# Kernel tuning notes

Hardware: AMD Instinct MI355X
Metric: run time of the kernel (lower is better)

Reference implementation:

```python
import jax, jax.numpy as jnp
import numpy as np

B, C, H, W = 4, 256, 128, 128
K = 3
BN = max(16, C // 4)  # 64
PAD = K // 2
EPS = 1e-5


def conv2d(x, w, b=None, pad=0):
    out = jax.lax.conv_general_dilated(
        x, w, (1, 1), [(pad, pad), (pad, pad)],
        dimension_numbers=("NCHW", "OIHW", "NCHW"))
    if b is not None:
        out = out + b[None, :, None, None]
    return out


def deform_conv2d(z, offset, mask, w, b):
    # torchvision modulated deform conv v2: offset [B,2*K*K,H,W] interleaved (dy,dx),
    # mask [B,K*K,H,W], kernel positions row-major, stride 1, pad PAD.
    Bz, Cb, Hz, Wz = z.shape
    K2 = K * K
    off = offset.reshape(Bz, K2, 2, Hz, Wz)
    ky, kx = jnp.meshgrid(jnp.arange(K), jnp.arange(K), indexing="ij")
    # sampling positions py/px: [B, K2, H, W]
    py = off[:, :, 0] + jnp.arange(Hz)[None, None, :, None] + (ky.reshape(K2) - PAD)[None, :, None, None]
    px = off[:, :, 1] + jnp.arange(Wz)[None, None, None, :] + (kx.reshape(K2) - PAD)[None, :, None, None]
    y0 = jnp.floor(py)
    x0 = jnp.floor(px)
    wy1 = py - y0  # frac weights
    wx1 = px - x0
    z_flat = z.reshape(Bz, Cb, Hz * Wz)

    def gather(yy, xx, wgt):
        valid = (yy >= 0) & (yy < Hz) & (xx >= 0) & (xx < Wz)
        yc = jnp.clip(yy, 0, Hz - 1).astype(jnp.int32)
        xc = jnp.clip(xx, 0, Wz - 1).astype(jnp.int32)
        idx = (yc * Wz + xc).reshape(Bz, K2 * Hz * Wz)
        g = jnp.take_along_axis(z_flat, idx[:, None, :], axis=2)  # [B, Cb, K2*H*W]
        g = g.reshape(Bz, Cb, K2, Hz, Wz)
        return g * (wgt * valid.astype(z.dtype))[:, None]

    val = (gather(y0, x0, (1 - wy1) * (1 - wx1))
           + gather(y0, x0 + 1, (1 - wy1) * wx1)
           + gather(y0 + 1, x0, wy1 * (1 - wx1))
           + gather(y0 + 1, x0 + 1, wy1 * wx1))
    val = val * mask[:, None]  # modulate: [B, Cb, K2, H, W]
    out = jnp.einsum("bckhw,ock->bohw", val, w.reshape(w.shape[0], Cb, K2))
    return out + b[None, :, None, None]


def setup_inputs() -> dict:
    key = jax.random.key(0)
    ks = jax.random.split(key, 11)
    s = 0.05
    return {
        "x": jax.random.normal(ks[0], (B, C, H, W), jnp.float32),
        "down_w": jax.random.normal(ks[1], (BN, C, 1, 1), jnp.float32) * s,
        "off_w": jax.random.normal(ks[2], (2 * K * K, BN, 3, 3), jnp.float32) * s,
        "off_b": jax.random.normal(ks[3], (2 * K * K,), jnp.float32) * s,
        "mask_w": jax.random.normal(ks[4], (K * K, BN, 3, 3), jnp.float32) * s,
        "mask_b": jax.random.normal(ks[5], (K * K,), jnp.float32) * s,
        "def_w": jax.random.normal(ks[6], (BN, BN, K, K), jnp.float32) * s,
        "def_b": jax.random.normal(ks[7], (BN,), jnp.float32) * s,
        "up_w": jax.random.normal(ks[8], (C, BN, 1, 1), jnp.float32) * s,
        "gamma": jnp.ones((C,), jnp.float32),
        "beta": jnp.zeros((C,), jnp.float32),
    }


def reference(x, down_w, off_w, off_b, mask_w, mask_b, def_w, def_b, up_w, gamma, beta):
    z = conv2d(x, down_w)                               # 1x1 down: [B, BN, H, W]
    offset = conv2d(z, off_w, off_b, pad=1)             # [B, 18, H, W]
    mask = jax.nn.sigmoid(conv2d(z, mask_w, mask_b, pad=1))  # [B, 9, H, W]
    z = deform_conv2d(z, offset, mask, def_w, def_b)    # [B, BN, H, W]
    z = conv2d(z, up_w)                                 # 1x1 up: [B, C, H, W]
    y = x + z
    # BatchNorm2d in training mode: batch statistics over (B, H, W), biased var
    mean = jnp.mean(y, axis=(0, 2, 3), keepdims=True)
    var = jnp.var(y, axis=(0, 2, 3), keepdims=True)
    yh = (y - mean) * jax.lax.rsqrt(var + EPS)
    yh = yh * gamma[None, :, None, None] + beta[None, :, None, None]
    return yh * jax.nn.sigmoid(yh)  # SiLU
```

## Files before the change

### kernel.cpp

```cpp
#include <hip/hip_runtime.h>
#include <hip/hip_bf16.h>


typedef __attribute__((ext_vector_type(8))) short bf16x8;
typedef __attribute__((ext_vector_type(4))) short bf16x4;
typedef __attribute__((ext_vector_type(4))) float f32x4;

#define HW   16384
#define CC   256
#define BNC  64

#define WS_STATS   0
#define WS_SS      262144
#define WS_FD      264192
#define WS_FOM     296960
#define WS_FDEF    333824
#define WS_FUP     407552
#define WS_ZBF     440320
#define WS_OM      8828928

__device__ __forceinline__ short f2b(float f) {
    unsigned u = __float_as_uint(f);
    unsigned r = (u + 0x7FFFu + ((u >> 16) & 1u)) >> 16;
    return (short)r;
}
__device__ __forceinline__ float b2f(short s) {
    return __uint_as_float(((unsigned)(unsigned short)s) << 16);
}

__global__ void k_prep(const float* __restrict__ down_w, const float* __restrict__ off_w,
                       const float* __restrict__ mask_w, const float* __restrict__ def_w,
                       const float* __restrict__ up_w, char* __restrict__ ws) {
    int g = blockIdx.x * 256 + threadIdx.x;
    int row = g >> 6, lane = g & 63;
    if (row >= 172) return;
    int l15 = lane & 15, q = lane >> 4;
    short vals[8];
    short* dst;
    if (row < 32) {
        int nt = row >> 3, kk = row & 7;
        int n = nt * 16 + l15;
        for (int j = 0; j < 8; ++j) {
            int c = kk * 32 + q * 8 + j;
            vals[j] = f2b(down_w[n * 256 + c]);
        }
        dst = (short*)(ws + WS_FD) + row * 512 + lane * 8;
    } else if (row < 68) {
        int r = row - 32; int nt = r / 18, kk = r % 18;
        int n = nt * 16 + l15;
        for (int j = 0; j < 8; ++j) {
            int kap = kk * 32 + q * 8 + j; int k = kap >> 6, c = kap & 63;
            float v = 0.f;
            if (n < 18)      v = off_w[(n * 64 + c) * 9 + k];
            else if (n < 27) v = mask_w[((n - 18) * 64 + c) * 9 + k];
            vals[j] = f2b(v);
        }
        dst = (short*)(ws + WS_FOM) + r * 512 + lane * 8;
    } else if (row < 140) {
        int r = row - 68; int nt = r / 18, kk = r % 18;
        int n = nt * 16 + l15;
        int u = kk * 4 + q, k = u >> 3;
        for (int j = 0; j < 8; ++j) {
            int c = (u & 7) * 8 + j;
            vals[j] = f2b(def_w[(n * 64 + c) * 9 + k]);
        }
        dst = (short*)(ws + WS_FDEF) + r * 512 + lane * 8;
    } else {
        int r = row - 140; int nt = r >> 1, kk = r & 1;
        int o = nt * 16 + l15;
        for (int j = 0; j < 8; ++j) {
            int c = kk * 32 + q * 8 + j;
            vals[j] = f2b(up_w[o * 64 + c]);
        }
        dst = (short*)(ws + WS_FUP) + r * 512 + lane * 8;
    }
    for (int j = 0; j < 8; ++j) dst[j] = vals[j];
}

__global__ __launch_bounds__(256) void k_down(const float* __restrict__ x,
                                              const short* __restrict__ wfd,
                                              short* __restrict__ zbf) {
    __shared__ __align__(16) short xl[64 * 264];
    int blk = blockIdx.x;
    int b = blk >> 8;
    int hw0 = (blk & 255) * 64;
    int t = threadIdx.x;
    const float* xb = x + (size_t)b * CC * HW + hw0;
    int px = t & 63, w = t >> 6;
    for (int h = 0; h < 8; ++h) {
        int c0 = h * 32 + w * 8;
        bf16x8 pk;
        #pragma unroll
        for (int j = 0; j < 8; ++j)
            pk[j] = f2b(xb[(size_t)(c0 + j) * HW + px]);
        *(bf16x8*)(&xl[px * 264 + c0]) = pk;
    }
    __syncthreads();
    int lane = t & 63, wv = t >> 6;
    int l15 = lane & 15, q = lane >> 4;
    bf16x8 A[8];
    const short* xrow = &xl[(wv * 16 + l15) * 264];
    for (int kk = 0; kk < 8; ++kk)
        A[kk] = *(const bf16x8*)(xrow + kk * 32 + q * 8);
    const bf16x8* Bp = (const bf16x8*)wfd;
    size_t obase = ((size_t)b * HW + hw0 + wv * 16) * 64;
    for (int nt = 0; nt < 4; ++nt) {
        f32x4 acc = {0.f, 0.f, 0.f, 0.f};
        for (int kk = 0; kk < 8; ++kk) {
            bf16x8 Bf = Bp[(nt * 8 + kk) * 64 + lane];
            acc = __builtin_amdgcn_mfma_f32_16x16x32_bf16(A[kk], Bf, acc, 0, 0, 0);
        }
        int n = nt * 16 + l15;
        for (int r = 0; r < 4; ++r) {
            int prow = q * 4 + r;
            zbf[obase + (size_t)prow * 64 + n] = f2b(acc[r]);
        }
    }
}

__global__ __launch_bounds__(256) void k_offmask(const short* __restrict__ zbf,
                                                 const short* __restrict__ wfom,
                                                 const float* __restrict__ off_b,
                                                 const float* __restrict__ mask_b,
                                                 float* __restrict__ om) {
    int blk = blockIdx.x;
    int b = blk >> 8;
    int hw0 = (blk & 255) * 64;
    int y = hw0 >> 7, x0 = hw0 & 127;
    int t = threadIdx.x, lane = t & 63, wv = t >> 6;
    int l15 = lane & 15, q = lane >> 4;
    int xx0 = x0 + wv * 16 + l15;
    const short* zb = zbf + (size_t)b * HW * 64;
    f32x4 acc0 = {0, 0, 0, 0}, acc1 = {0, 0, 0, 0};
    const bf16x8* Bp = (const bf16x8*)wfom;
    for (int kk = 0; kk < 18; ++kk) {
        int k = kk >> 1;
        int yy = y + (k / 3) - 1;
        int xx = xx0 + (k % 3) - 1;
        int c0 = (kk & 1) * 32 + q * 8;
        bf16x8 A = {0, 0, 0, 0, 0, 0, 0, 0};
        if (yy >= 0 && yy < 128 && xx >= 0 && xx < 128)
            A = *(const bf16x8*)(zb + ((size_t)(yy * 128 + xx)) * 64 + c0);
        bf16x8 B0 = Bp[kk * 64 + lane];
        bf16x8 B1 = Bp[(18 + kk) * 64 + lane];
        acc0 = __builtin_amdgcn_mfma_f32_16x16x32_bf16(A, B0, acc0, 0, 0, 0);
        acc1 = __builtin_amdgcn_mfma_f32_16x16x32_bf16(A, B1, acc1, 0, 0, 0);
    }
    float* omb = om + ((size_t)b * HW + hw0 + wv * 16) * 27;
    for (int half = 0; half < 2; ++half) {
        f32x4 acc = half ? acc1 : acc0;
        int n = half * 16 + l15;
        if (n < 27) {
            for (int r = 0; r < 4; ++r) {
                int prow = q * 4 + r;
                float v = acc[r];
                if (n < 18) v += off_b[n];
                else { v += mask_b[n - 18]; v = 1.f / (1.f + __expf(-v)); }
                omb[prow * 27 + n] = v;
            }
        }
    }
}

__global__ __launch_bounds__(256) void k_deform_up(
        const short* __restrict__ zbf, const float* __restrict__ om,
        const short* __restrict__ wfdef, const float* __restrict__ def_b,
        const short* __restrict__ wfup, const float* __restrict__ x,
        float* __restrict__ yout, float* __restrict__ stats) {
    __shared__ __align__(16) short valA[1152 * 8];
    __shared__ __align__(16) char  uSm[4608];
    int4*   pAi4 = (int4*)uSm;
    float4* pAw4 = (float4*)(uSm + 2304);
    short*  z2t  = (short*)uSm;

    int blk = blockIdx.x;
    int b = blk >> 10;
    int tile = blk & 1023;
    int oy = tile >> 3, xt = (tile & 7) << 4;
    int hw0 = oy * 128 + xt;
    int t = threadIdx.x;
    const short* zbs = zbf + (size_t)b * HW * 64;
    if (t < 144) {
        int px = t / 9, k = t % 9;
        int ox = xt + px;
        const float* p = om + ((size_t)b * HW + hw0 + px) * 27;
        float dy = p[2 * k], dx = p[2 * k + 1], m = p[18 + k];
        float py  = (float)oy + (float)(k / 3 - 1) + dy;
        float pxf = (float)ox + (float)(k % 3 - 1) + dx;
        float fy = floorf(py), fx = floorf(pxf);
        int iy = (int)fy, ix = (int)fx;
        float wy = py - fy, wx = pxf - fx;
        float ww[4] = { (1.f - wy) * (1.f - wx) * m, (1.f - wy) * wx * m,
                        wy * (1.f - wx) * m,          wy * wx * m };
        int ys[2] = {iy, iy + 1}, xs[2] = {ix, ix + 1};
        int   ri[4]; float rw[4];
        for (int ci = 0; ci < 4; ++ci) {
            int cy = ys[ci >> 1], cx = xs[ci & 1];
            bool v = (cy >= 0 && cy < 128 && cx >= 0 && cx < 128);
            ri[ci] = v ? (cy * 128 + cx) * 64 : 0;
            rw[ci] = v ? ww[ci] : 0.f;
        }
        pAi4[t] = make_int4(ri[0], ri[1], ri[2], ri[3]);
        pAw4[t] = make_float4(rw[0], rw[1], rw[2], rw[3]);
    }
    __syncthreads();
    for (int it = 0; it < 5; ++it) {
        int s = t + it * 256;
        if (s < 1152) {
            int px = s / 72;
            int u  = s - px * 72;
            int k = u >> 3, cg = u & 7;
            int task = px * 9 + k;
            int4   idx = pAi4[task];
            float4 wt  = pAw4[task];
            int   ii[4] = { idx.x, idx.y, idx.z, idx.w };
            float wwt[4] = { wt.x, wt.y, wt.z, wt.w };
            int cgs = cg * 8;
            float acc[8] = {0.f, 0.f, 0.f, 0.f, 0.f, 0.f, 0.f, 0.f};
            #pragma unroll
            for (int ci = 0; ci < 4; ++ci) {
                float w = wwt[ci];
                int4 d = *(const int4*)(zbs + ii[ci] + cgs);
                int dp[4] = { d.x, d.y, d.z, d.w };
                #pragma unroll
                for (int p = 0; p < 4; ++p) {
                    float lo = __uint_as_float((unsigned)dp[p] << 16);
                    float hi = __uint_as_float((unsigned)dp[p] & 0xffff0000u);
                    acc[2 * p]     += w * lo;
                    acc[2 * p + 1] += w * hi;
                }
            }
            bf16x8 out;
            #pragma unroll
            for (int j = 0; j < 8; ++j) out[j] = f2b(acc[j]);
            int unit = u * 16 + (px ^ (u & 15));
            *(bf16x8*)(&valA[unit * 8]) = out;
        }
    }
    __syncthreads();
    int lane = t & 63, wv = t >> 6;
    int l15 = lane & 15, q = lane >> 4;
    {
        f32x4 acc = {0, 0, 0, 0};
        const bf16x8* Bp = (const bf16x8*)wfdef;
        for (int kk = 0; kk < 18; ++kk) {
            int u = kk * 4 + q;
            int unit = u * 16 + (l15 ^ (u & 15));
            bf16x8 A  = *(const bf16x8*)(&valA[unit * 8]);
            bf16x8 Bf = Bp[(wv * 18 + kk) * 64 + lane];
            acc = __builtin_amdgcn_mfma_f32_16x16x32_bf16(A, Bf, acc, 0, 0, 0);
        }
        int n = wv * 16 + l15;
        float bias = def_b[n];
        for (int r = 0; r < 4; ++r) {
            int prow = q * 4 + r;
            z2t[prow * 64 + (n ^ ((prow & 7) << 3))] = f2b(acc[r] + bias);
        }
    }
    __syncthreads();
    int rsw = (l15 & 7) << 3;
    bf16x8 A0 = *(const bf16x8*)&z2t[l15 * 64 + ((q * 8) ^ rsw)];
    bf16x8 A1 = *(const bf16x8*)&z2t[l15 * 64 + ((32 + q * 8) ^ rsw)];
    const bf16x8* Bu = (const bf16x8*)wfup;
    int bucket = blk & 127;
    size_t xybase = (size_t)b * CC * HW + hw0 + q * 4;
    #pragma unroll
    for (int nt = 0; nt < 4; ++nt) {
        int ont = wv * 4 + nt;
        f32x4 acc = {0, 0, 0, 0};
        acc = __builtin_amdgcn_mfma_f32_16x16x32_bf16(A0, Bu[(ont * 2 + 0) * 64 + lane], acc, 0, 0, 0);
        acc = __builtin_amdgcn_mfma_f32_16x16x32_bf16(A1, Bu[(ont * 2 + 1) * 64 + lane], acc, 0, 0, 0);
        int o = ont * 16 + l15;
        size_t pb = xybase + (size_t)o * HW;
        float4 xv = *(const float4*)(x + pb);
        float v0 = acc[0] + xv.x;
        float v1 = acc[1] + xv.y;
        float v2 = acc[2] + xv.z;
        float v3 = acc[3] + xv.w;
        *(float4*)(yout + pb) = make_float4(v0, v1, v2, v3);
        float s  = v0 + v1 + v2 + v3;
        float s2 = v0 * v0 + v1 * v1 + v2 * v2 + v3 * v3;
        s  += __shfl_xor(s, 16);  s  += __shfl_xor(s, 32);
        s2 += __shfl_xor(s2, 16); s2 += __shfl_xor(s2, 32);
        if (q == 0) {
            atomicAdd(&stats[bucket * 512 + o], s);
            atomicAdd(&stats[bucket * 512 + 256 + o], s2);
        }
    }
}

__global__ void k_stats(const float* __restrict__ stats, const float* __restrict__ gamma,
                        const float* __restrict__ beta, float* __restrict__ ss) {
    int o = threadIdx.x;
    float a0 = 0.f, a1 = 0.f, a2 = 0.f, a3 = 0.f;
    float b0 = 0.f, b1 = 0.f, b2 = 0.f, b3 = 0.f;
    #pragma unroll 4
    for (int u = 0; u < 128; u += 4) {
        a0 += stats[(u + 0) * 512 + o];  b0 += stats[(u + 0) * 512 + 256 + o];
        a1 += stats[(u + 1) * 512 + o];  b1 += stats[(u + 1) * 512 + 256 + o];
        a2 += stats[(u + 2) * 512 + o];  b2 += stats[(u + 2) * 512 + 256 + o];
        a3 += stats[(u + 3) * 512 + o];  b3 += stats[(u + 3) * 512 + 256 + o];
    }
    float s = (a0 + a1) + (a2 + a3);
    float s2 = (b0 + b1) + (b2 + b3);
    float mean = s * (1.f / 65536.f);
    float var  = s2 * (1.f / 65536.f) - mean * mean;
    float rs = rsqrtf(var + 1e-5f);
    float sc = gamma[o] * rs;
    ss[o]       = sc;
    ss[256 + o] = beta[o] - mean * sc;
}

__global__ __launch_bounds__(256) void k_bn(float* __restrict__ y, const float* __restrict__ ss) {
    int g = blockIdx.x * 256 + threadIdx.x;
    int o = (g >> 10) & 255;
    float sc = ss[o], sh = ss[256 + o];
    float4* p = (float4*)y + (size_t)g * 4;
    for (int i = 0; i < 4; ++i) {
        float4 v = p[i];
        float vf[4] = { v.x, v.y, v.z, v.w };
        for (int j = 0; j < 4; ++j) {
            float h = vf[j] * sc + sh;
            vf[j] = h / (1.f + __expf(-h));
        }
        p[i] = make_float4(vf[0], vf[1], vf[2], vf[3]);
    }
}

extern "C" void kernel_launch(void* const* d_in, const int* in_sizes, int n_in,
                              void* d_out, int out_size, void* d_ws, size_t ws_size,
                              hipStream_t stream) {
    const float* x      = (const float*)d_in[0];
    const float* down_w = (const float*)d_in[1];
    const float* off_w  = (const float*)d_in[2];
    const float* off_b  = (const float*)d_in[3];
    const float* mask_w = (const float*)d_in[4];
    const float* mask_b = (const float*)d_in[5];
    const float* def_w  = (const float*)d_in[6];
    const float* def_b  = (const float*)d_in[7];
    const float* up_w   = (const float*)d_in[8];
    const float* gamma  = (const float*)d_in[9];
    const float* beta   = (const float*)d_in[10];
    char* ws = (char*)d_ws;
    float* stats = (float*)(ws + WS_STATS);
    float* ss    = (float*)(ws + WS_SS);
    short* wfd   = (short*)(ws + WS_FD);
    short* wfom  = (short*)(ws + WS_FOM);
    short* wfdef = (short*)(ws + WS_FDEF);
    short* wfup  = (short*)(ws + WS_FUP);
    short* zbf   = (short*)(ws + WS_ZBF);
    float* om    = (float*)(ws + WS_OM);
    float* y     = (float*)d_out;

    hipMemsetAsync(stats, 0, 128 * 512 * sizeof(float), stream);
    hipLaunchKernelGGL(k_prep,      dim3(43),   dim3(256), 0, stream, down_w, off_w, mask_w, def_w, up_w, ws);
    hipLaunchKernelGGL(k_down,      dim3(1024), dim3(256), 0, stream, x, wfd, zbf);
    hipLaunchKernelGGL(k_offmask,   dim3(1024), dim3(256), 0, stream, zbf, wfom, off_b, mask_b, om);
    hipLaunchKernelGGL(k_deform_up, dim3(4096), dim3(256), 0, stream, zbf, om, wfdef, def_b, wfup, x, y, stats);
    hipLaunchKernelGGL(k_stats,     dim3(1),    dim3(256), 0, stream, stats, gamma, beta, ss);
    hipLaunchKernelGGL(k_bn,        dim3(4096), dim3(256), 0, stream, y, ss);
}
```

Measured before the change: 230.1 us.

## Enlarge deform+up tile to 64 pixels per block with sequential sub-tiles

Each k_deform_up block now covers 64 consecutive pixels of a row instead of 16. It runs the sampling, gather and deform MFMA phases over four 16-pixel sub-tiles, stores all results into a 64x64 z2t buffer, then does the 1x1 up-projection over four row tiles. The grid drops from 4096 to 1024 blocks. The aim is to amortise block launch, weight fragment loads and per-block setup over more pixels and to give longer contiguous x/y row accesses. The costs are less parallelism, more LDS per block because buffers are no longer aliased, and serialised barriers within each block that may reduce latency hiding.

Result: slower. 244.4 us (+6.2%).

```diff
diff --git a/kernel.cpp b/kernel.cpp
--- a/kernel.cpp
+++ b/kernel.cpp
@@ -167,124 +167,130 @@
         const short* __restrict__ wfdef, const float* __restrict__ def_b,
         const short* __restrict__ wfup, const float* __restrict__ x,
         float* __restrict__ yout, float* __restrict__ stats) {
-    __shared__ __align__(16) short valA[1152 * 8];
-    __shared__ __align__(16) char  uSm[4608];
-    int4*   pAi4 = (int4*)uSm;
-    float4* pAw4 = (float4*)(uSm + 2304);
-    short*  z2t  = (short*)uSm;
+    __shared__ __align__(16) short  valA[1152 * 8];
+    __shared__ __align__(16) short  z2t[64 * 64];
+    __shared__ __align__(16) int4   pAi4[144];
+    __shared__ __align__(16) float4 pAw4[144];
 
     int blk = blockIdx.x;
-    int b = blk >> 10;
-    int tile = blk & 1023;
-    int oy = tile >> 3, xt = (tile & 7) << 4;
-    int hw0 = oy * 128 + xt;
+    int b = blk >> 8;
+    int tile = blk & 255;
+    int oy = tile >> 1;
+    int x0 = (tile & 1) << 6;
+    int hw0 = oy * 128 + x0;
     int t = threadIdx.x;
-    const short* zbs = zbf + (size_t)b * HW * 64;
-    if (t < 144) {
-        int px = t / 9, k = t % 9;
-        int ox = xt + px;
-        const float* p = om + ((size_t)b * HW + hw0 + px) * 27;
-        float dy = p[2 * k], dx = p[2 * k + 1], m = p[18 + k];
-        float py  = (float)oy + (float)(k / 3 - 1) + dy;
-        float pxf = (float)ox + (float)(k % 3 - 1) + dx;
-        float fy = floorf(py), fx = floorf(pxf);
-        int iy = (int)fy, ix = (int)fx;
-        float wy = py - fy, wx = pxf - fx;
-        float ww[4] = { (1.f - wy) * (1.f - wx) * m, (1.f - wy) * wx * m,
-                        wy * (1.f - wx) * m,          wy * wx * m };
-        int ys[2] = {iy, iy + 1}, xs[2] = {ix, ix + 1};
-        int   ri[4]; float rw[4];
-        for (int ci = 0; ci < 4; ++ci) {
-            int cy = ys[ci >> 1], cx = xs[ci & 1];
-            bool v = (cy >= 0 && cy < 128 && cx >= 0 && cx < 128);
-            ri[ci] = v ? (cy * 128 + cx) * 64 : 0;
-            rw[ci] = v ? ww[ci] : 0.f;
-        }
-        pAi4[t] = make_int4(ri[0], ri[1], ri[2], ri[3]);
-        pAw4[t] = make_float4(rw[0], rw[1], rw[2], rw[3]);
-    }
-    __syncthreads();
-    for (int it = 0; it < 5; ++it) {
-        int s = t + it * 256;
-        if (s < 1152) {
-            int px = s / 72;
-            int u  = s - px * 72;
-            int k = u >> 3, cg = u & 7;
-            int task = px * 9 + k;
-            int4   idx = pAi4[task];
-            float4 wt  = pAw4[task];
-            int   ii[4] = { idx.x, idx.y, idx.z, idx.w };
-            float wwt[4] = { wt.x, wt.y, wt.z, wt.w };
-            int cgs = cg * 8;
-            float acc[8] = {0.f, 0.f, 0.f, 0.f, 0.f, 0.f, 0.f, 0.f};
-            #pragma unroll
-            for (int ci = 0; ci < 4; ++ci) {
-                float w = wwt[ci];
-                int4 d = *(const int4*)(zbs + ii[ci] + cgs);
-                int dp[4] = { d.x, d.y, d.z, d.w };
-                #pragma unroll
-                for (int p = 0; p < 4; ++p) {
-                    float lo = __uint_as_float((unsigned)dp[p] << 16);
-                    float hi = __uint_as_float((unsigned)dp[p] & 0xffff0000u);
-                    acc[2 * p]     += w * lo;
-                    acc[2 * p + 1] += w * hi;
-                }
-            }
-            bf16x8 out;
-            #pragma unroll
-            for (int j = 0; j < 8; ++j) out[j] = f2b(acc[j]);
-            int unit = u * 16 + (px ^ (u & 15));
-            *(bf16x8*)(&valA[unit * 8]) = out;
-        }
-    }
-    __syncthreads();
     int lane = t & 63, wv = t >> 6;
     int l15 = lane & 15, q = lane >> 4;
-    {
-        f32x4 acc = {0, 0, 0, 0};
-        const bf16x8* Bp = (const bf16x8*)wfdef;
-        for (int kk = 0; kk < 18; ++kk) {
-            int u = kk * 4 + q;
-            int unit = u * 16 + (l15 ^ (u & 15));
-            bf16x8 A  = *(const bf16x8*)(&valA[unit * 8]);
-            bf16x8 Bf = Bp[(wv * 18 + kk) * 64 + lane];
-            acc = __builtin_amdgcn_mfma_f32_16x16x32_bf16(A, Bf, acc, 0, 0, 0);
-        }
-        int n = wv * 16 + l15;
-        float bias = def_b[n];
-        for (int r = 0; r < 4; ++r) {
-            int prow = q * 4 + r;
-            z2t[prow * 64 + (n ^ ((prow & 7) << 3))] = f2b(acc[r] + bias);
+    const short* zbs = zbf + (size_t)b * HW * 64;
+    const bf16x8* Bp = (const bf16x8*)wfdef;
+
+    for (int st = 0; st < 4; ++st) {
+        if (t < 144) {
+            int px = t / 9, k = t % 9;
+            int ox = x0 + st * 16 + px;
+            const float* p = om + ((size_t)b * HW + oy * 128 + ox) * 27;
+            float dy = p[2 * k], dx = p[2 * k + 1], m = p[18 + k];
+            float py  = (float)oy + (float)(k / 3 - 1) + dy;
+            float pxf = (float)ox + (float)(k % 3 - 1) + dx;
+            float fy = floorf(py), fx = floorf(pxf);
+            int iy = (int)fy, ix = (int)fx;
+            float wy = py - fy, wx = pxf - fx;
+            float ww[4] = { (1.f - wy) * (1.f - wx) * m, (1.f - wy) * wx * m,
+                            wy * (1.f - wx) * m,          wy * wx * m };
+            int ys[2] = {iy, iy + 1}, xs[2] = {ix, ix + 1};
+            int   ri[4]; float rw[4];
+            for (int ci = 0; ci < 4; ++ci) {
+                int cy = ys[ci >> 1], cx = xs[ci & 1];
+                bool v = (cy >= 0 && cy < 128 && cx >= 0 && cx < 128);
+                ri[ci] = v ? (cy * 128 + cx) * 64 : 0;
+                rw[ci] = v ? ww[ci] : 0.f;
+            }
+            pAi4[t] = make_int4(ri[0], ri[1], ri[2], ri[3]);
+            pAw4[t] = make_float4(rw[0], rw[1], rw[2], rw[3]);
+        }
+        __syncthreads();
+        for (int it = 0; it < 5; ++it) {
+            int s = t + it * 256;
+            if (s < 1152) {
+                int px = s / 72;
+                int u  = s - px * 72;
+                int cg = u & 7;
+                int task = px * 9 + (u >> 3);
+                int4   idx = pAi4[task];
+                float4 wt  = pAw4[task];
+                int   ii[4] = { idx.x, idx.y, idx.z, idx.w };
+                float wwt[4] = { wt.x, wt.y, wt.z, wt.w };
+                int cgs = cg * 8;
+                float acc[8] = {0.f, 0.f, 0.f, 0.f, 0.f, 0.f, 0.f, 0.f};
+                #pragma unroll
+                for (int ci = 0; ci < 4; ++ci) {
+                    float w = wwt[ci];
+                    int4 d = *(const int4*)(zbs + ii[ci] + cgs);
+                    int dp[4] = { d.x, d.y, d.z, d.w };
+                    #pragma unroll
+                    for (int p = 0; p < 4; ++p) {
+                        float lo = __uint_as_float((unsigned)dp[p] << 16);
+                        float hi = __uint_as_float((unsigned)dp[p] & 0xffff0000u);
+                        acc[2 * p]     += w * lo;
+                        acc[2 * p + 1] += w * hi;
+                    }
+                }
+                bf16x8 out;
+                #pragma unroll
+                for (int j = 0; j < 8; ++j) out[j] = f2b(acc[j]);
+                int unit = u * 16 + (px ^ (u & 15));
+                *(bf16x8*)(&valA[unit * 8]) = out;
+            }
+        }
+        __syncthreads();
+        {
+            f32x4 acc = {0, 0, 0, 0};
+            for (int kk = 0; kk < 18; ++kk) {
+                int u = kk * 4 + q;
+                int unit = u * 16 + (l15 ^ (u & 15));
+                bf16x8 A  = *(const bf16x8*)(&valA[unit * 8]);
+                bf16x8 Bf = Bp[(wv * 18 + kk) * 64 + lane];
+                acc = __builtin_amdgcn_mfma_f32_16x16x32_bf16(A, Bf, acc, 0, 0, 0);
+            }
+            int n = wv * 16 + l15;
+            float bias = def_b[n];
+            for (int r = 0; r < 4; ++r) {
+                int prow = st * 16 + q * 4 + r;
+                z2t[prow * 64 + (n ^ ((prow & 7) << 3))] = f2b(acc[r] + bias);
+            }
         }
     }
     __syncthreads();
-    int rsw = (l15 & 7) << 3;
-    bf16x8 A0 = *(const bf16x8*)&z2t[l15 * 64 + ((q * 8) ^ rsw)];
-    bf16x8 A1 = *(const bf16x8*)&z2t[l15 * 64 + ((32 + q * 8) ^ rsw)];
     const bf16x8* Bu = (const bf16x8*)wfup;
     int bucket = blk & 127;
     size_t xybase = (size_t)b * CC * HW + hw0 + q * 4;
-    #pragma unroll
-    for (int nt = 0; nt < 4; ++nt) {
-        int ont = wv * 4 + nt;
-        f32x4 acc = {0, 0, 0, 0};
-        acc = __builtin_amdgcn_mfma_f32_16x16x32_bf16(A0, Bu[(ont * 2 + 0) * 64 + lane], acc, 0, 0, 0);
-        acc = __builtin_amdgcn_mfma_f32_16x16x32_bf16(A1, Bu[(ont * 2 + 1) * 64 + lane], acc, 0, 0, 0);
-        int o = ont * 16 + l15;
-        size_t pb = xybase + (size_t)o * HW;
-        float4 xv = *(const float4*)(x + pb);
-        float v0 = acc[0] + xv.x;
-        float v1 = acc[1] + xv.y;
-        float v2 = acc[2] + xv.z;
-        float v3 = acc[3] + xv.w;
-        *(float4*)(yout + pb) = make_float4(v0, v1, v2, v3);
-        float s  = v0 + v1 + v2 + v3;
-        float s2 = v0 * v0 + v1 * v1 + v2 * v2 + v3 * v3;
-        s  += __shfl_xor(s, 16);  s  += __shfl_xor(s, 32);
-        s2 += __shfl_xor(s2, 16); s2 += __shfl_xor(s2, 32);
-        if (q == 0) {
-            atomicAdd(&stats[bucket * 512 + o], s);
-            atomicAdd(&stats[bucket * 512 + 256 + o], s2);
+    for (int mt = 0; mt < 4; ++mt) {
+        int arow = mt * 16 + l15;
+        int rsw = (arow & 7) << 3;
+        bf16x8 A0 = *(const bf16x8*)&z2t[arow * 64 + ((q * 8) ^ rsw)];
+        bf16x8 A1 = *(const bf16x8*)&z2t[arow * 64 + ((32 + q * 8) ^ rsw)];
+        #pragma unroll
+        for (int nt = 0; nt < 4; ++nt) {
+            int ont = wv * 4 + nt;
+            f32x4 acc = {0, 0, 0, 0};
+            acc = __builtin_amdgcn_mfma_f32_16x16x32_bf16(A0, Bu[(ont * 2 + 0) * 64 + lane], acc, 0, 0, 0);
+            acc = __builtin_amdgcn_mfma_f32_16x16x32_bf16(A1, Bu[(ont * 2 + 1) * 64 + lane], acc, 0, 0, 0);
+            int o = ont * 16 + l15;
+            size_t pb = xybase + (size_t)o * HW + mt * 16;
+            float4 xv = *(const float4*)(x + pb);
+            float v0 = acc[0] + xv.x;
+            float v1 = acc[1] + xv.y;
+            float v2 = acc[2] + xv.z;
+            float v3 = acc[3] + xv.w;
+            *(float4*)(yout + pb) = make_float4(v0, v1, v2, v3);
+            float s  = v0 + v1 + v2 + v3;
+            float s2 = v0 * v0 + v1 * v1 + v2 * v2 + v3 * v3;
+            s  += __shfl_xor(s, 16);  s  += __shfl_xor(s, 32);
+            s2 += __shfl_xor(s2, 16); s2 += __shfl_xor(s2, 32);
+            if (q == 0) {
+                atomicAdd(&stats[bucket * 512 + o], s);
+                atomicAdd(&stats[bucket * 512 + 256 + o], s2);
+            }
         }
     }
 }
@@ -356,7 +362,7 @@
     hipLaunchKernelGGL(k_prep,      dim3(43),   dim3(256), 0, stream, down_w, off_w, mask_w, def_w, up_w, ws);
     hipLaunchKernelGGL(k_down,      dim3(1024), dim3(256), 0, stream, x, wfd, zbf);
     hipLaunchKernelGGL(k_offmask,   dim3(1024), dim3(256), 0, stream, zbf, wfom, off_b, mask_b, om);
-    hipLaunchKernelGGL(k_deform_up, dim3(4096), dim3(256), 0, stream, zbf, om, wfdef, def_b, wfup, x, y, stats);
+    hipLaunchKernelGGL(k_deform_up, dim3(1024), dim3(256), 0, stream, zbf, om, wfdef, def_b, wfup, x, y, stats);
     hipLaunchKernelGGL(k_stats,     dim3(1),    dim3(256), 0, stream, stats, gamma, beta, ss);
     hipLaunchKernelGGL(k_bn,        dim3(4096), dim3(256), 0, stream, y, ss);
 }
```
